# Kernel optimization log

Measured on AMD Instinct MI355X. Metric: run time of the kernel, lower is better.

## Reference

```python
import jax, jax.numpy as jnp
import numpy as np


def setup_inputs() -> dict:
    key = jax.random.key(0)
    ks = jax.random.split(key, 5)
    B, T, C, H, E = 8, 2048, 1024, 2048, 8
    n_layer = 12
    x = jax.random.normal(ks[0], (B, T, C), dtype=jnp.float32)
    w_router = jax.random.normal(ks[1], (C, E), dtype=jnp.float32) * 0.02
    w_c_fc = jax.random.normal(ks[2], (E, C, H), dtype=jnp.float32) * 0.02
    w_gate = jax.random.normal(ks[3], (E, C, H), dtype=jnp.float32) * 0.02
    w_c_proj = jax.random.normal(ks[4], (E, H, C), dtype=jnp.float32) * (0.02 * (2 * n_layer) ** -0.5)
    return {
        "x": x, "w_router": w_router, "w_c_fc": w_c_fc,
        "w_gate": w_gate, "w_c_proj": w_c_proj,
        "top_k": 2, "n_experts": E, "expert_capacity": 640,
    }


def reference(x, w_router, w_c_fc, w_gate, w_c_proj, top_k, n_experts, expert_capacity):
    B, T, C = x.shape
    # ---- router ----
    gate_logits = jnp.einsum('btc,ce->bte', x, w_router)
    gate_probs = jax.nn.softmax(gate_logits, axis=-1)  # (B,T,E)

    # ---- per-batch top-k dispatch (cumsum slot assignment + scatter) ----
    def dispatch(xb, pb):
        # xb: (T,C), pb: (T,E)
        topk_p, topk_i = jax.lax.top_k(pb, top_k)              # (T,k)
        ei = jnp.swapaxes(topk_i, 0, 1).ravel()                # (k*T,) k-major
        oh = jax.nn.one_hot(ei, n_experts, dtype=jnp.int32)    # (k*T,E)
        pos = jnp.cumsum(oh, axis=0) * oh - 1                  # slot within expert
        pos = jnp.swapaxes(pos.reshape(top_k, T, n_experts), 0, 1).max(axis=2)  # (T,k)
        ei = jnp.swapaxes(ei.reshape(top_k, T), 0, 1)          # (T,k)
        buf = jnp.zeros((n_experts, expert_capacity, C), dtype=xb.dtype)
        xr = jnp.repeat(xb, top_k, axis=0)                     # (T*k,C) token-major
        buf = buf.at[ei.ravel(), pos.ravel()].set(xr)          # overflow slots dropped
        return topk_p, pos, ei, buf

    topk_p, pos, ei, buf = jax.vmap(dispatch)(x, gate_probs)   # buf: (B,E,cap,C)

    # ---- batched expert SwiGLU GEMMs ----
    ein = jnp.swapaxes(buf, 0, 1).reshape(n_experts, B * expert_capacity, C)
    h = jnp.einsum('eti,eih->eth', ein, w_c_fc)
    g = jax.nn.silu(jnp.einsum('eti,eih->eth', ein, w_gate))
    o = jnp.einsum('eth,eho->eto', g * h, w_c_proj)
    eo = jnp.swapaxes(o.reshape(n_experts, B, expert_capacity, C), 0, 1)  # (B,E,cap,C)

    # ---- weighted combine gather ----
    def combine(eo_b, i_b, p_b, pr_b):
        sel = eo_b[i_b, p_b]                                   # (T,k,C)
        return jnp.sum(pr_b[..., None] * sel, axis=1)          # (T,C)

    y = jax.vmap(combine)(eo, ei, pos, topk_p)                 # (B,T,C)
    return y
```

## Files before the change

### kernel.cpp

```cpp
#include <hip/hip_runtime.h>
#include <stdint.h>

#define B_   8
#define T_   2048
#define C_   1024
#define H_   2048
#define E_   8
#define CAP_ 640
#define RPE_ (B_*CAP_)
#define BT_  (B_*T_)
#define NE_  2

typedef __attribute__((ext_vector_type(8))) short bf16x8;
typedef __attribute__((ext_vector_type(4))) float f32x4;

static __device__ __forceinline__ unsigned short f2bf(float f){
  union { float f; uint32_t u; } a; a.f = f;
  uint32_t u = a.u;
  uint32_t r = (u + 0x7FFFu + ((u >> 16) & 1u)) >> 16;
  return (unsigned short)r;
}

#define GLD16(gp, lp) __builtin_amdgcn_global_load_lds( \
    (__attribute__((address_space(1))) void*)(gp), \
    (__attribute__((address_space(3))) void*)(lp), 16, 0, 0)

#define SBAR0 __builtin_amdgcn_sched_barrier(0)

#define PHASE(s, vm) do { \
    asm volatile("s_waitcnt vmcnt(" #vm ")" ::: "memory"); \
    SBAR0; \
    __builtin_amdgcn_s_barrier(); \
    SBAR0; \
    COMPUTE(s); \
    SBAR0; \
    __builtin_amdgcn_s_barrier(); \
    SBAR0; \
  } while(0)

__global__ __launch_bounds__(256) void router_kernel(
    const float* __restrict__ x, const float* __restrict__ wr,
    unsigned short* __restrict__ xbf, float* __restrict__ probs2, int* __restrict__ idx2)
{
  int bt = blockIdx.x;
  int tid = threadIdx.x;
  const float4 v = ((const float4*)(x + (size_t)bt*C_))[tid];
  ushort4 u;
  u.x = f2bf(v.x); u.y = f2bf(v.y); u.z = f2bf(v.z); u.w = f2bf(v.w);
  ((ushort4*)(xbf + (size_t)bt*C_))[tid] = u;

  double p[8];
  #pragma unroll
  for (int e=0;e<8;e++) p[e]=0.0;
  const float xv[4] = {v.x, v.y, v.z, v.w};
  #pragma unroll
  for (int j=0;j<4;j++){
    int c = tid*4+j;
    const float* wrow = wr + c*8;
    #pragma unroll
    for (int e=0;e<8;e++) p[e] += (double)xv[j] * (double)wrow[e];
  }
  __shared__ double red[8][256];
  #pragma unroll
  for (int e=0;e<8;e++) red[e][tid] = p[e];
  __syncthreads();
  for (int s=128; s>0; s>>=1){
    if (tid < s){
      #pragma unroll
      for (int e=0;e<8;e++) red[e][tid] += red[e][tid+s];
    }
    __syncthreads();
  }
  if (tid==0){
    double lg[8];
    #pragma unroll
    for (int e=0;e<8;e++) lg[e]=red[e][0];
    double mx = lg[0];
    #pragma unroll
    for (int e=1;e<8;e++) if (lg[e]>mx) mx=lg[e];
    double s=0.0, ex[8];
    #pragma unroll
    for (int e=0;e<8;e++){ ex[e]=exp(lg[e]-mx); s+=ex[e]; }
    int i1=0; double b1=ex[0];
    #pragma unroll
    for (int e=1;e<8;e++) if (ex[e]>b1){ b1=ex[e]; i1=e; }
    int i2=-1; double b2=-1.0;
    #pragma unroll
    for (int e=0;e<8;e++) if (e!=i1 && ex[e]>b2){ b2=ex[e]; i2=e; }
    probs2[bt*2+0] = (float)(b1/s);
    probs2[bt*2+1] = (float)(b2/s);
    idx2[bt*2+0] = i1;
    idx2[bt*2+1] = i2;
  }
}

__global__ __launch_bounds__(256) void transp_fcg_kernel(
    const float* __restrict__ fc, const float* __restrict__ gate,
    unsigned short* __restrict__ dst)
{
  __shared__ float t[32][33];
  int e = blockIdx.z;
  int n0 = blockIdx.x*32, k0 = blockIdx.y*32;
  int tx = threadIdx.x & 31, ty = threadIdx.x >> 5;
  #pragma unroll
  for (int sel=0; sel<2; ++sel){
    const float* s = (sel ? gate : fc) + ((size_t)e*C_ + k0)*H_ + n0;
    #pragma unroll
    for (int i=0;i<32;i+=8) t[ty+i][tx] = s[(size_t)(ty+i)*H_ + tx];
    __syncthreads();
    #pragma unroll
    for (int i=0;i<32;i+=8){
      int jj = ty+i;
      int drow = n0*2 + ((jj & 16) << 1) + sel*16 + (jj & 15);
      dst[((size_t)e*4096 + drow)*1024 + k0 + tx] = f2bf(t[tx][jj]);
    }
    __syncthreads();
  }
}

__global__ __launch_bounds__(256) void transp_kernel(
    const float* __restrict__ src, unsigned short* __restrict__ dst, int K, int N)
{
  __shared__ float t[32][33];
  int e = blockIdx.z;
  int n0 = blockIdx.x*32, k0 = blockIdx.y*32;
  int tx = threadIdx.x & 31, ty = threadIdx.x >> 5;
  const float* s = src + ((size_t)e*K + k0)*N + n0;
  #pragma unroll
  for (int i=0;i<32;i+=8) t[ty+i][tx] = s[(size_t)(ty+i)*N + tx];
  __syncthreads();
  unsigned short* d = dst + ((size_t)e*N + n0)*K + k0;
  #pragma unroll
  for (int i=0;i<32;i+=8) d[(size_t)(ty+i)*K + tx] = f2bf(t[tx][ty+i]);
}

__global__ void scan_kernel(const int* __restrict__ idx2, int* __restrict__ pos, int* __restrict__ cnt)
{
  int b = blockIdx.x, lane = threadIdx.x;
  unsigned long long below = (lane == 0) ? 0ull : (~0ull >> (64 - lane));
  int base = 0;
  for (int k=0;k<2;k++){
    for (int c0=0;c0<T_;c0+=64){
      int t = c0 + lane;
      int e = idx2[((b*T_ + t)<<1) + k];
      unsigned long long mym = 0; int addv = 0;
      #pragma unroll
      for (int ee=0; ee<8; ++ee){
        unsigned long long m = __ballot(e == ee);
        if (ee == e) mym = m;
        if (lane == ee) addv = __popcll(m);
      }
      int mybase = __shfl(base, e, 64);
      pos[((b*T_+t)<<1)+k] = mybase + __popcll(mym & below);
      base += addv;
    }
  }
  if (lane < 8) cnt[b*8 + lane] = (base < CAP_) ? base : CAP_;
}

__global__ void offsets_kernel(const int* __restrict__ cnt, int* __restrict__ off, int* __restrict__ Me)
{
  int e = threadIdx.x;
  if (e < 8){
    int s = 0;
    for (int b=0;b<8;b++){ off[e*8+b] = s; s += cnt[b*8+e]; }
    Me[e] = s;
  }
}

__global__ void fill_kernel(const int* __restrict__ idx2, const int* __restrict__ pos,
                            const int* __restrict__ off, const float* __restrict__ probs2,
                            int* __restrict__ token_src, float* __restrict__ row_prob)
{
  int a = blockIdx.x*256 + threadIdx.x;
  if (a >= BT_*2) return;
  int bt = a >> 1, k = a & 1;
  int b = bt >> 11;
  int e = idx2[bt*2+k];
  int p = pos[bt*2+k];
  if (p < CAP_){
    int r = e*RPE_ + off[e*8+b] + p;
    token_src[r] = bt;
    row_prob[r] = probs2[bt*2+k];
  }
}

__global__ __launch_bounds__(256) void gemm1_kernel(
    const unsigned short* __restrict__ xbf,
    const unsigned short* __restrict__ wifcg,
    const int* __restrict__ token_src,
    const int* __restrict__ Me,
    unsigned short* __restrict__ act,
    int e0)
{
  const int ez = blockIdx.z, e = e0 + ez, mt = blockIdx.y, nt = blockIdx.x;
  const int M = Me[e];
  if (mt*128 >= M) return;

  __shared__ __align__(16) unsigned char lds[65536];

  const int tid = threadIdx.x;
  const int w = tid >> 6, l = tid & 63;
  const int wrow = w >> 1, wcol = w & 1;

  size_t aBase[2], bBase[2];
  #pragma unroll
  for (int j=0;j<2;++j){
    int idx = j*256 + tid;
    int r = idx >> 2, c = idx & 3;
    int sc = c ^ ((r >> 1) & 3);
    int tok = token_src[e*RPE_ + mt*128 + r];
    aBase[j] = (size_t)tok*2048u + (unsigned)(sc*16);
    bBase[j] = ((size_t)(ez*4096 + nt*128 + r))*2048u + (unsigned)(sc*16);
  }
  const unsigned char* gA = (const unsigned char*)xbf;
  const unsigned char* gB = (const unsigned char*)wifcg;

  unsigned rdA[4], rdB[4];
  const int g = l >> 4;
  #pragma unroll
  for (int f=0; f<4; ++f){
    int ra = wrow*64 + f*16 + (l & 15);
    rdA[f] = (unsigned)(ra*64 + ((g ^ ((ra>>1)&3)) << 4));
    int rb = wcol*64 + f*16 + (l & 15);
    rdB[f] = (unsigned)(32768 + rb*64 + ((g ^ ((rb>>1)&3)) << 4));
  }

  f32x4 acc[4][4];
  #pragma unroll
  for (int i=0;i<4;i++)
    #pragma unroll
    for (int j=0;j<4;j++) acc[i][j] = (f32x4){0.f,0.f,0.f,0.f};

  #define STAGE(s) do { \
    unsigned slot_ = ((unsigned)(s)&3u)*8192u; \
    unsigned kb_ = (unsigned)(s)*64u; \
    GLD16(gA + aBase[0] + kb_, lds + slot_ + 0*4096 + w*1024); \
    GLD16(gA + aBase[1] + kb_, lds + slot_ + 1*4096 + w*1024); \
    GLD16(gB + bBase[0] + kb_, lds + 32768 + slot_ + 0*4096 + w*1024); \
    GLD16(gB + bBase[1] + kb_, lds + 32768 + slot_ + 1*4096 + w*1024); \
  } while(0)

  #define COMPUTE(s) do { \
    unsigned slot_ = ((unsigned)(s)&3u)*8192u; \
    bf16x8 afr[4], bfr[4]; \
    _Pragma("unroll") \
    for (int f=0; f<4; ++f) afr[f] = *(const bf16x8*)(lds + slot_ + rdA[f]); \
    _Pragma("unroll") \
    for (int f=0; f<4; ++f) bfr[f] = *(const bf16x8*)(lds + slot_ + rdB[f]); \
    __builtin_amdgcn_s_setprio(1); \
    _Pragma("unroll") \
    for (int fm=0; fm<4; ++fm) \
      _Pragma("unroll") \
      for (int fn=0; fn<4; ++fn) \
        acc[fm][fn] = __builtin_amdgcn_mfma_f32_16x16x32_bf16(afr[fm], bfr[fn], acc[fm][fn], 0,0,0); \
    __builtin_amdgcn_s_setprio(0); \
  } while(0)

  STAGE(0); STAGE(1); STAGE(2);
  for (int s = 0; s < 29; ++s){
    STAGE(s+3);
    PHASE(s, 12);
  }
  PHASE(29, 8);
  PHASE(30, 4);
  PHASE(31, 0);

  #undef STAGE
  #undef COMPUTE

  #pragma unroll
  for (int fm=0; fm<4; ++fm){
    #pragma unroll
    for (int t=0; t<2; ++t){
      f32x4 h = acc[fm][2*t], gg = acc[fm][2*t+1];
      #pragma unroll
      for (int r=0; r<4; ++r){
        int row = mt*128 + wrow*64 + fm*16 + (l>>4)*4 + r;
        int col = nt*64 + wcol*32 + t*16 + (l & 15);
        float gv = gg[r];
        float a = (gv / (1.f + __expf(-gv))) * h[r];
        act[((size_t)ez*RPE_ + row)*(size_t)H_ + col] = f2bf(a);
      }
    }
  }
}

__global__ __launch_bounds__(256) void gemm2_kernel(
    const unsigned short* __restrict__ act,
    const unsigned short* __restrict__ wprojT,
    const int* __restrict__ token_src,
    const float* __restrict__ row_prob,
    const int* __restrict__ Me,
    float* __restrict__ y,
    int e0)
{
  const int ez = blockIdx.z, e = e0 + ez, mt = blockIdx.y, nt = blockIdx.x;
  const int M = Me[e];
  if (mt*128 >= M) return;

  __shared__ __align__(16) unsigned char lds[65536];

  const int tid = threadIdx.x;
  const int w = tid >> 6, l = tid & 63;
  const int wrow = w >> 1, wcol = w & 1;

  size_t aBase[2], bBase[2];
  #pragma unroll
  for (int j=0;j<2;++j){
    int idx = j*256 + tid;
    int r = idx >> 2, c = idx & 3;
    int sc = c ^ ((r >> 1) & 3);
    aBase[j] = ((size_t)(ez*RPE_ + mt*128 + r))*4096u + (unsigned)(sc*16);
    bBase[j] = ((size_t)(ez*C_ + nt*128 + r))*4096u + (unsigned)(sc*16);
  }
  const unsigned char* gA = (const unsigned char*)act;
  const unsigned char* gB = (const unsigned char*)wprojT;

  unsigned rdA[4], rdB[4];
  const int g = l >> 4;
  #pragma unroll
  for (int f=0; f<4; ++f){
    int ra = wrow*64 + f*16 + (l & 15);
    rdA[f] = (unsigned)(ra*64 + ((g ^ ((ra>>1)&3)) << 4));
    int rb = wcol*64 + f*16 + (l & 15);
    rdB[f] = (unsigned)(32768 + rb*64 + ((g ^ ((rb>>1)&3)) << 4));
  }

  f32x4 acc[4][4];
  #pragma unroll
  for (int i=0;i<4;i++)
    #pragma unroll
    for (int j=0;j<4;j++) acc[i][j] = (f32x4){0.f,0.f,0.f,0.f};

  #define STAGE(s) do { \
    unsigned slot_ = ((unsigned)(s)&3u)*8192u; \
    unsigned kb_ = (unsigned)(s)*64u; \
    GLD16(gA + aBase[0] + kb_, lds + slot_ + 0*4096 + w*1024); \
    GLD16(gA + aBase[1] + kb_, lds + slot_ + 1*4096 + w*1024); \
    GLD16(gB + bBase[0] + kb_, lds + 32768 + slot_ + 0*4096 + w*1024); \
    GLD16(gB + bBase[1] + kb_, lds + 32768 + slot_ + 1*4096 + w*1024); \
  } while(0)

  #define COMPUTE(s) do { \
    unsigned slot_ = ((unsigned)(s)&3u)*8192u; \
    bf16x8 afr[4], bfr[4]; \
    _Pragma("unroll") \
    for (int f=0; f<4; ++f) afr[f] = *(const bf16x8*)(lds + slot_ + rdA[f]); \
    _Pragma("unroll") \
    for (int f=0; f<4; ++f) bfr[f] = *(const bf16x8*)(lds + slot_ + rdB[f]); \
    __builtin_amdgcn_s_setprio(1); \
    _Pragma("unroll") \
    for (int fm=0; fm<4; ++fm) \
      _Pragma("unroll") \
      for (int fn=0; fn<4; ++fn) \
        acc[fm][fn] = __builtin_amdgcn_mfma_f32_16x16x32_bf16(afr[fm], bfr[fn], acc[fm][fn], 0,0,0); \
    __builtin_amdgcn_s_setprio(0); \
  } while(0)

  STAGE(0); STAGE(1); STAGE(2);
  for (int s = 0; s < 61; ++s){
    STAGE(s+3);
    PHASE(s, 12);
  }
  PHASE(61, 8);
  PHASE(62, 4);
  PHASE(63, 0);

  #undef STAGE
  #undef COMPUTE

  #pragma unroll
  for (int fm=0; fm<4; ++fm){
    #pragma unroll
    for (int r=0; r<4; ++r){
      int rloc = mt*128 + wrow*64 + fm*16 + (l>>4)*4 + r;
      if (rloc < M){
        int bt  = token_src[e*RPE_ + rloc];
        float p = row_prob[e*RPE_ + rloc];
        float* yrow = y + (size_t)bt*C_;
        #pragma unroll
        for (int fn=0; fn<4; ++fn){
          int col = nt*128 + wcol*64 + fn*16 + (l & 15);
          atomicAdd(yrow + col, p * acc[fm][fn][r]);
        }
      }
    }
  }
}

extern "C" void kernel_launch(void* const* d_in, const int* in_sizes, int n_in,
                              void* d_out, int out_size, void* d_ws, size_t ws_size,
                              hipStream_t stream)
{
  const float* x   = (const float*)d_in[0];
  const float* wr  = (const float*)d_in[1];
  const float* wfc = (const float*)d_in[2];
  const float* wg  = (const float*)d_in[3];
  const float* wpj = (const float*)d_in[4];
  float* y = (float*)d_out;

  unsigned char* ws = (unsigned char*)d_ws;
  const size_t szXBF  = (size_t)BT_*C_*2;
  const size_t szFCGc = (size_t)NE_*4096*1024*2;
  const size_t szWPc  = (size_t)NE_*C_*H_*2;
  const size_t szFCGa = (size_t)E_*4096*1024*2;
  const size_t szWPa  = (size_t)E_*C_*H_*2;
  const size_t szACT  = (size_t)NE_*RPE_*H_*2;
  const size_t szMISC = 3*131072 + 2*(size_t)E_*RPE_*4 + 1024;

  const size_t need_small = szXBF + szFCGc + szWPc + szACT + szMISC;
  const size_t need_big   = szXBF + szFCGa + szWPa + szACT + szMISC;
  if (ws_size < need_small) return;
  const bool big = (ws_size >= need_big);

  const size_t szFCG = big ? szFCGa : szFCGc;
  const size_t szWP  = big ? szWPa  : szWPc;

  size_t oXBF = 0;
  size_t oFCG = oXBF + szXBF;
  size_t oWP  = oFCG + szFCG;
  size_t oACT = oWP  + szWP;
  size_t oM   = oACT + szACT;

  unsigned short* xbf    = (unsigned short*)(ws + oXBF);
  unsigned short* wifcg  = (unsigned short*)(ws + oFCG);
  unsigned short* wprojT = (unsigned short*)(ws + oWP);
  unsigned short* actc   = (unsigned short*)(ws + oACT);

  float* probs2    = (float*)(ws + oM);
  int*   idx2      = (int*)(ws + oM + 1*131072);
  int*   pos       = (int*)(ws + oM + 2*131072);
  int*   token_src = (int*)(ws + oM + 3*131072);
  float* row_prob  = (float*)(ws + oM + 3*131072 + (size_t)E_*RPE_*4);
  int*   cnt       = (int*)(ws + oM + 3*131072 + 2*(size_t)E_*RPE_*4);
  int*   off       = cnt + 64;
  int*   Me        = off + 64;

  hipMemsetAsync(y, 0, (size_t)out_size*4, stream);
  hipMemsetAsync(token_src, 0, (size_t)E_*RPE_*4, stream);

  router_kernel<<<BT_, 256, 0, stream>>>(x, wr, xbf, probs2, idx2);
  scan_kernel<<<B_, 64, 0, stream>>>(idx2, pos, cnt);
  offsets_kernel<<<1, 64, 0, stream>>>(cnt, off, Me);
  fill_kernel<<<(BT_*2+255)/256, 256, 0, stream>>>(idx2, pos, off, probs2, token_src, row_prob);

  if (big){
    transp_fcg_kernel<<<dim3(H_/32, C_/32, E_), 256, 0, stream>>>(wfc, wg, wifcg);
    transp_kernel<<<dim3(C_/32, H_/32, E_), 256, 0, stream>>>(wpj, wprojT, H_, C_);
  }

  for (int e0 = 0; e0 < E_; e0 += NE_){
    unsigned short* wfcg_c = wifcg;
    unsigned short* wpj_c  = wprojT;
    if (big){
      wfcg_c = wifcg  + (size_t)e0*4096*1024;
      wpj_c  = wprojT + (size_t)e0*C_*H_;
    } else {
      transp_fcg_kernel<<<dim3(H_/32, C_/32, NE_), 256, 0, stream>>>(
          wfc + (size_t)e0*C_*H_, wg + (size_t)e0*C_*H_, wifcg);
      transp_kernel<<<dim3(C_/32, H_/32, NE_), 256, 0, stream>>>(
          wpj + (size_t)e0*H_*C_, wprojT, H_, C_);
    }
    gemm1_kernel<<<dim3(4096/128, RPE_/128, NE_), 256, 0, stream>>>(
        xbf, wfcg_c, token_src, Me, actc, e0);
    gemm2_kernel<<<dim3(C_/128, RPE_/128, NE_), 256, 0, stream>>>(
        actc, wpj_c, token_src, row_prob, Me, y, e0);
  }
}
```

Before: 900.0 us.

## Enlarge expert GEMM tiles to 256x256 with 8 waves and double-buffered LDS

Both expert GEMM kernels move from 128x128 tiles with 4 waves and a 4-slot BK=32 ring to 256x256 tiles with 8 waves, BK=64 and two 64KB LDS buffers. Each K-step is split into four quadrant phases that interleave the next tile's loads with MFMA work. The goal is more operand reuse per byte loaded and less barrier overhead per MFMA. In exchange it uses 128KB of LDS and many more accumulator registers per block, which may limit occupancy and leave partially filled M tiles on experts with few tokens.

```diff
diff --git a/kernel.cpp b/kernel.cpp
--- a/kernel.cpp
+++ b/kernel.cpp
@@ -25,18 +25,53 @@
     (__attribute__((address_space(1))) void*)(gp), \
     (__attribute__((address_space(3))) void*)(lp), 16, 0, 0)
 
-#define SBAR0 __builtin_amdgcn_sched_barrier(0)
-
-#define PHASE(s, vm) do { \
-    asm volatile("s_waitcnt vmcnt(" #vm ")" ::: "memory"); \
-    SBAR0; \
-    __builtin_amdgcn_s_barrier(); \
-    SBAR0; \
-    COMPUTE(s); \
-    SBAR0; \
-    __builtin_amdgcn_s_barrier(); \
-    SBAR0; \
-  } while(0)
+#define VMW(N) asm volatile("s_waitcnt vmcnt(" #N ")" ::: "memory")
+#define FENCE  asm volatile("" ::: "memory")
+
+#define PHASE(AH, BH, STG_STMT, WAIT_STMT) do { \
+  bf16x8 afr[2][4], bfr[2][2]; \
+  _Pragma("unroll") \
+  for (int ks=0; ks<2; ++ks){ \
+    _Pragma("unroll") \
+    for (int f=0; f<4; ++f) \
+      afr[ks][f] = *(const bf16x8*)(bufc + (AH)*16384u + aRow + (unsigned)f*2048u + cc[ks]); \
+    _Pragma("unroll") \
+    for (int n=0; n<2; ++n) \
+      bfr[ks][n] = *(const bf16x8*)(bufc + 32768u + (BH)*16384u + bRow + (unsigned)n*2048u + cc[ks]); \
+  } \
+  STG_STMT; \
+  WAIT_STMT; \
+  FENCE; \
+  __builtin_amdgcn_s_barrier(); \
+  __builtin_amdgcn_sched_barrier(0); \
+  __builtin_amdgcn_s_setprio(1); \
+  _Pragma("unroll") \
+  for (int ks=0; ks<2; ++ks) \
+    _Pragma("unroll") \
+    for (int f=0; f<4; ++f) \
+      _Pragma("unroll") \
+      for (int n=0; n<2; ++n) \
+        acc[(AH)*2+(BH)][f][n] = __builtin_amdgcn_mfma_f32_16x16x32_bf16( \
+            afr[ks][f], bfr[ks][n], acc[(AH)*2+(BH)][f][n], 0,0,0); \
+  __builtin_amdgcn_s_setprio(0); \
+  __builtin_amdgcn_sched_barrier(0); \
+  FENCE; \
+  __builtin_amdgcn_s_barrier(); \
+  FENCE; \
+} while(0)
+
+#define STG_A(H, T1) do { \
+  unsigned kb_ = (unsigned)(T1)*128u; \
+  unsigned db_ = ((unsigned)(T1)&1u)*65536u + (H)*16384u; \
+  GLD16(pA##H##0 + kb_, lds + db_ + d0); \
+  GLD16(pA##H##1 + kb_, lds + db_ + 8192u + d0); \
+} while(0)
+#define STG_B(H, T1) do { \
+  unsigned kb_ = (unsigned)(T1)*128u; \
+  unsigned db_ = ((unsigned)(T1)&1u)*65536u + 32768u + (H)*16384u; \
+  GLD16(pB##H##0 + kb_, lds + db_ + d0); \
+  GLD16(pB##H##1 + kb_, lds + db_ + 8192u + d0); \
+} while(0)
 
 __global__ __launch_bounds__(256) void router_kernel(
     const float* __restrict__ x, const float* __restrict__ wr,
@@ -185,7 +220,7 @@
   }
 }
 
-__global__ __launch_bounds__(256) void gemm1_kernel(
+__global__ __launch_bounds__(512, 2) void gemm1_kernel(
     const unsigned short* __restrict__ xbf,
     const unsigned short* __restrict__ wifcg,
     const int* __restrict__ token_src,
@@ -195,98 +230,85 @@
 {
   const int ez = blockIdx.z, e = e0 + ez, mt = blockIdx.y, nt = blockIdx.x;
   const int M = Me[e];
-  if (mt*128 >= M) return;
-
-  __shared__ __align__(16) unsigned char lds[65536];
+  if (mt*256 >= M) return;
+
+  __shared__ __align__(16) unsigned char lds[131072];
 
   const int tid = threadIdx.x;
   const int w = tid >> 6, l = tid & 63;
-  const int wrow = w >> 1, wcol = w & 1;
-
-  size_t aBase[2], bBase[2];
-  #pragma unroll
-  for (int j=0;j<2;++j){
-    int idx = j*256 + tid;
-    int r = idx >> 2, c = idx & 3;
-    int sc = c ^ ((r >> 1) & 3);
-    int tok = token_src[e*RPE_ + mt*128 + r];
-    aBase[j] = (size_t)tok*2048u + (unsigned)(sc*16);
-    bBase[j] = ((size_t)(ez*4096 + nt*128 + r))*2048u + (unsigned)(sc*16);
-  }
+  const int wm = w >> 2, wn = w & 3;
+  const int l15 = l & 15, g0 = l >> 4;
+  const unsigned d0 = (unsigned)tid * 16u;
+
+  const int srow0 = tid >> 3, c0 = tid & 7;
+  const unsigned scb = (unsigned)((c0 ^ (srow0 & 7)) * 16);
   const unsigned char* gA = (const unsigned char*)xbf;
   const unsigned char* gB = (const unsigned char*)wifcg;
-
-  unsigned rdA[4], rdB[4];
-  const int g = l >> 4;
-  #pragma unroll
-  for (int f=0; f<4; ++f){
-    int ra = wrow*64 + f*16 + (l & 15);
-    rdA[f] = (unsigned)(ra*64 + ((g ^ ((ra>>1)&3)) << 4));
-    int rb = wcol*64 + f*16 + (l & 15);
-    rdB[f] = (unsigned)(32768 + rb*64 + ((g ^ ((rb>>1)&3)) << 4));
-  }
-
-  f32x4 acc[4][4];
-  #pragma unroll
-  for (int i=0;i<4;i++)
-    #pragma unroll
-    for (int j=0;j<4;j++) acc[i][j] = (f32x4){0.f,0.f,0.f,0.f};
-
-  #define STAGE(s) do { \
-    unsigned slot_ = ((unsigned)(s)&3u)*8192u; \
-    unsigned kb_ = (unsigned)(s)*64u; \
-    GLD16(gA + aBase[0] + kb_, lds + slot_ + 0*4096 + w*1024); \
-    GLD16(gA + aBase[1] + kb_, lds + slot_ + 1*4096 + w*1024); \
-    GLD16(gB + bBase[0] + kb_, lds + 32768 + slot_ + 0*4096 + w*1024); \
-    GLD16(gB + bBase[1] + kb_, lds + 32768 + slot_ + 1*4096 + w*1024); \
-  } while(0)
-
-  #define COMPUTE(s) do { \
-    unsigned slot_ = ((unsigned)(s)&3u)*8192u; \
-    bf16x8 afr[4], bfr[4]; \
-    _Pragma("unroll") \
-    for (int f=0; f<4; ++f) afr[f] = *(const bf16x8*)(lds + slot_ + rdA[f]); \
-    _Pragma("unroll") \
-    for (int f=0; f<4; ++f) bfr[f] = *(const bf16x8*)(lds + slot_ + rdB[f]); \
-    __builtin_amdgcn_s_setprio(1); \
-    _Pragma("unroll") \
-    for (int fm=0; fm<4; ++fm) \
-      _Pragma("unroll") \
-      for (int fn=0; fn<4; ++fn) \
-        acc[fm][fn] = __builtin_amdgcn_mfma_f32_16x16x32_bf16(afr[fm], bfr[fn], acc[fm][fn], 0,0,0); \
-    __builtin_amdgcn_s_setprio(0); \
-  } while(0)
-
-  STAGE(0); STAGE(1); STAGE(2);
-  for (int s = 0; s < 29; ++s){
-    STAGE(s+3);
-    PHASE(s, 12);
-  }
-  PHASE(29, 8);
-  PHASE(30, 4);
-  PHASE(31, 0);
-
-  #undef STAGE
-  #undef COMPUTE
-
-  #pragma unroll
-  for (int fm=0; fm<4; ++fm){
-    #pragma unroll
-    for (int t=0; t<2; ++t){
-      f32x4 h = acc[fm][2*t], gg = acc[fm][2*t+1];
-      #pragma unroll
-      for (int r=0; r<4; ++r){
-        int row = mt*128 + wrow*64 + fm*16 + (l>>4)*4 + r;
-        int col = nt*64 + wcol*32 + t*16 + (l & 15);
-        float gv = gg[r];
-        float a = (gv / (1.f + __expf(-gv))) * h[r];
-        act[((size_t)ez*RPE_ + row)*(size_t)H_ + col] = f2bf(a);
+  const int abase = e*RPE_ + mt*256;
+  const unsigned char* pA00 = gA + (size_t)token_src[abase +       srow0]*2048u + scb;
+  const unsigned char* pA01 = gA + (size_t)token_src[abase +  64 + srow0]*2048u + scb;
+  const unsigned char* pA10 = gA + (size_t)token_src[abase + 128 + srow0]*2048u + scb;
+  const unsigned char* pA11 = gA + (size_t)token_src[abase + 192 + srow0]*2048u + scb;
+  const size_t bbase = (size_t)(ez*4096 + nt*256 + srow0);
+  const unsigned char* pB00 = gB + (bbase +   0)*2048u + scb;
+  const unsigned char* pB01 = gB + (bbase +  64)*2048u + scb;
+  const unsigned char* pB10 = gB + (bbase + 128)*2048u + scb;
+  const unsigned char* pB11 = gB + (bbase + 192)*2048u + scb;
+
+  const unsigned aRow = (unsigned)((wm*64 + l15) * 128);
+  const unsigned bRow = (unsigned)((wn*32 + l15) * 128);
+  unsigned cc[2];
+  cc[0] = (unsigned)(((0*4 + g0) ^ (l15 & 7)) * 16);
+  cc[1] = (unsigned)(((1*4 + g0) ^ (l15 & 7)) * 16);
+
+  f32x4 acc[4][4][2];
+  #pragma unroll
+  for (int p=0;p<4;++p)
+    #pragma unroll
+    for (int f=0;f<4;++f)
+      #pragma unroll
+      for (int n=0;n<2;++n) acc[p][f][n] = (f32x4){0.f,0.f,0.f,0.f};
+
+  STG_A(0,0); STG_B(0,0); STG_B(1,0); STG_A(1,0);
+  VMW(4);
+  FENCE; __builtin_amdgcn_s_barrier(); FENCE;
+
+  const int NT = 16;
+  for (int t = 0; t < NT-1; ++t){
+    const unsigned char* bufc = lds + (unsigned)(t&1)*65536u;
+    PHASE(0,0, STG_A(0,t+1), VMW(4));
+    PHASE(0,1, STG_B(0,t+1), VMW(4));
+    PHASE(1,0, STG_B(1,t+1), (void)0);
+    PHASE(1,1, STG_A(1,t+1), VMW(4));
+  }
+  {
+    const unsigned char* bufc = lds + (unsigned)((NT-1)&1)*65536u;
+    PHASE(0,0, (void)0, VMW(2));
+    PHASE(0,1, (void)0, VMW(0));
+    PHASE(1,0, (void)0, (void)0);
+    PHASE(1,1, (void)0, (void)0);
+  }
+
+  const int r4 = (l >> 4) * 4;
+  #pragma unroll
+  for (int p=0;p<4;++p){
+    const int ah = p>>1, bh = p&1;
+    #pragma unroll
+    for (int f=0;f<4;++f){
+      const int grow = mt*256 + ah*128 + wm*64 + f*16 + r4;
+      const int hcol = nt*128 + bh*64 + wn*16 + l15;
+      #pragma unroll
+      for (int r=0;r<4;++r){
+        float h = acc[p][f][0][r];
+        float gv = acc[p][f][1][r];
+        float a = (gv / (1.f + __expf(-gv))) * h;
+        act[((size_t)ez*RPE_ + grow + r)*(size_t)H_ + hcol] = f2bf(a);
       }
     }
   }
 }
 
-__global__ __launch_bounds__(256) void gemm2_kernel(
+__global__ __launch_bounds__(512, 2) void gemm2_kernel(
     const unsigned short* __restrict__ act,
     const unsigned short* __restrict__ wprojT,
     const int* __restrict__ token_src,
@@ -297,92 +319,81 @@
 {
   const int ez = blockIdx.z, e = e0 + ez, mt = blockIdx.y, nt = blockIdx.x;
   const int M = Me[e];
-  if (mt*128 >= M) return;
-
-  __shared__ __align__(16) unsigned char lds[65536];
+  if (mt*256 >= M) return;
+
+  __shared__ __align__(16) unsigned char lds[131072];
 
   const int tid = threadIdx.x;
   const int w = tid >> 6, l = tid & 63;
-  const int wrow = w >> 1, wcol = w & 1;
-
-  size_t aBase[2], bBase[2];
-  #pragma unroll
-  for (int j=0;j<2;++j){
-    int idx = j*256 + tid;
-    int r = idx >> 2, c = idx & 3;
-    int sc = c ^ ((r >> 1) & 3);
-    aBase[j] = ((size_t)(ez*RPE_ + mt*128 + r))*4096u + (unsigned)(sc*16);
-    bBase[j] = ((size_t)(ez*C_ + nt*128 + r))*4096u + (unsigned)(sc*16);
-  }
+  const int wm = w >> 2, wn = w & 3;
+  const int l15 = l & 15, g0 = l >> 4;
+  const unsigned d0 = (unsigned)tid * 16u;
+
+  const int srow0 = tid >> 3, c0 = tid & 7;
+  const unsigned scb = (unsigned)((c0 ^ (srow0 & 7)) * 16);
   const unsigned char* gA = (const unsigned char*)act;
   const unsigned char* gB = (const unsigned char*)wprojT;
-
-  unsigned rdA[4], rdB[4];
-  const int g = l >> 4;
-  #pragma unroll
-  for (int f=0; f<4; ++f){
-    int ra = wrow*64 + f*16 + (l & 15);
-    rdA[f] = (unsigned)(ra*64 + ((g ^ ((ra>>1)&3)) << 4));
-    int rb = wcol*64 + f*16 + (l & 15);
-    rdB[f] = (unsigned)(32768 + rb*64 + ((g ^ ((rb>>1)&3)) << 4));
-  }
-
-  f32x4 acc[4][4];
-  #pragma unroll
-  for (int i=0;i<4;i++)
-    #pragma unroll
-    for (int j=0;j<4;j++) acc[i][j] = (f32x4){0.f,0.f,0.f,0.f};
-
-  #define STAGE(s) do { \
-    unsigned slot_ = ((unsigned)(s)&3u)*8192u; \
-    unsigned kb_ = (unsigned)(s)*64u; \
-    GLD16(gA + aBase[0] + kb_, lds + slot_ + 0*4096 + w*1024); \
-    GLD16(gA + aBase[1] + kb_, lds + slot_ + 1*4096 + w*1024); \
-    GLD16(gB + bBase[0] + kb_, lds + 32768 + slot_ + 0*4096 + w*1024); \
-    GLD16(gB + bBase[1] + kb_, lds + 32768 + slot_ + 1*4096 + w*1024); \
-  } while(0)
-
-  #define COMPUTE(s) do { \
-    unsigned slot_ = ((unsigned)(s)&3u)*8192u; \
-    bf16x8 afr[4], bfr[4]; \
-    _Pragma("unroll") \
-    for (int f=0; f<4; ++f) afr[f] = *(const bf16x8*)(lds + slot_ + rdA[f]); \
-    _Pragma("unroll") \
-    for (int f=0; f<4; ++f) bfr[f] = *(const bf16x8*)(lds + slot_ + rdB[f]); \
-    __builtin_amdgcn_s_setprio(1); \
-    _Pragma("unroll") \
-    for (int fm=0; fm<4; ++fm) \
-      _Pragma("unroll") \
-      for (int fn=0; fn<4; ++fn) \
-        acc[fm][fn] = __builtin_amdgcn_mfma_f32_16x16x32_bf16(afr[fm], bfr[fn], acc[fm][fn], 0,0,0); \
-    __builtin_amdgcn_s_setprio(0); \
-  } while(0)
-
-  STAGE(0); STAGE(1); STAGE(2);
-  for (int s = 0; s < 61; ++s){
-    STAGE(s+3);
-    PHASE(s, 12);
-  }
-  PHASE(61, 8);
-  PHASE(62, 4);
-  PHASE(63, 0);
-
-  #undef STAGE
-  #undef COMPUTE
-
-  #pragma unroll
-  for (int fm=0; fm<4; ++fm){
-    #pragma unroll
-    for (int r=0; r<4; ++r){
-      int rloc = mt*128 + wrow*64 + fm*16 + (l>>4)*4 + r;
-      if (rloc < M){
-        int bt  = token_src[e*RPE_ + rloc];
-        float p = row_prob[e*RPE_ + rloc];
-        float* yrow = y + (size_t)bt*C_;
-        #pragma unroll
-        for (int fn=0; fn<4; ++fn){
-          int col = nt*128 + wcol*64 + fn*16 + (l & 15);
-          atomicAdd(yrow + col, p * acc[fm][fn][r]);
+  const size_t abase = (size_t)(ez*RPE_ + mt*256 + srow0);
+  const unsigned char* pA00 = gA + (abase +   0)*4096u + scb;
+  const unsigned char* pA01 = gA + (abase +  64)*4096u + scb;
+  const unsigned char* pA10 = gA + (abase + 128)*4096u + scb;
+  const unsigned char* pA11 = gA + (abase + 192)*4096u + scb;
+  const size_t bbase = (size_t)(ez*C_ + nt*256 + srow0);
+  const unsigned char* pB00 = gB + (bbase +   0)*4096u + scb;
+  const unsigned char* pB01 = gB + (bbase +  64)*4096u + scb;
+  const unsigned char* pB10 = gB + (bbase + 128)*4096u + scb;
+  const unsigned char* pB11 = gB + (bbase + 192)*4096u + scb;
+
+  const unsigned aRow = (unsigned)((wm*64 + l15) * 128);
+  const unsigned bRow = (unsigned)((wn*32 + l15) * 128);
+  unsigned cc[2];
+  cc[0] = (unsigned)(((0*4 + g0) ^ (l15 & 7)) * 16);
+  cc[1] = (unsigned)(((1*4 + g0) ^ (l15 & 7)) * 16);
+
+  f32x4 acc[4][4][2];
+  #pragma unroll
+  for (int p=0;p<4;++p)
+    #pragma unroll
+    for (int f=0;f<4;++f)
+      #pragma unroll
+      for (int n=0;n<2;++n) acc[p][f][n] = (f32x4){0.f,0.f,0.f,0.f};
+
+  STG_A(0,0); STG_B(0,0); STG_B(1,0); STG_A(1,0);
+  VMW(4);
+  FENCE; __builtin_amdgcn_s_barrier(); FENCE;
+
+  const int NT = 32;
+  for (int t = 0; t < NT-1; ++t){
+    const unsigned char* bufc = lds + (unsigned)(t&1)*65536u;
+    PHASE(0,0, STG_A(0,t+1), VMW(4));
+    PHASE(0,1, STG_B(0,t+1), VMW(4));
+    PHASE(1,0, STG_B(1,t+1), (void)0);
+    PHASE(1,1, STG_A(1,t+1), VMW(4));
+  }
+  {
+    const unsigned char* bufc = lds + (unsigned)((NT-1)&1)*65536u;
+    PHASE(0,0, (void)0, VMW(2));
+    PHASE(0,1, (void)0, VMW(0));
+    PHASE(1,0, (void)0, (void)0);
+    PHASE(1,1, (void)0, (void)0);
+  }
+
+  const int r4 = (l >> 4) * 4;
+  #pragma unroll
+  for (int p=0;p<4;++p){
+    const int ah = p>>1, bh = p&1;
+    #pragma unroll
+    for (int f=0;f<4;++f){
+      #pragma unroll
+      for (int r=0;r<4;++r){
+        const int rloc = mt*256 + ah*128 + wm*64 + f*16 + r4 + r;
+        if (rloc < M){
+          const int bt = token_src[e*RPE_ + rloc];
+          const float pp = row_prob[e*RPE_ + rloc];
+          float* yrow = y + (size_t)bt*C_;
+          const int colb = nt*256 + bh*128 + wn*32 + l15;
+          atomicAdd(yrow + colb,      pp * acc[p][f][0][r]);
+          atomicAdd(yrow + colb + 16, pp * acc[p][f][1][r]);
         }
       }
     }
@@ -462,9 +473,9 @@
       transp_kernel<<<dim3(C_/32, H_/32, NE_), 256, 0, stream>>>(
           wpj + (size_t)e0*H_*C_, wprojT, H_, C_);
     }
-    gemm1_kernel<<<dim3(4096/128, RPE_/128, NE_), 256, 0, stream>>>(
+    gemm1_kernel<<<dim3(4096/256, RPE_/256, NE_), 512, 0, stream>>>(
         xbf, wfcg_c, token_src, Me, actc, e0);
-    gemm2_kernel<<<dim3(C_/128, RPE_/128, NE_), 256, 0, stream>>>(
+    gemm2_kernel<<<dim3(C_/256, RPE_/256, NE_), 512, 0, stream>>>(
         actc, wpj_c, token_src, row_prob, Me, y, e0);
   }
 }
```

Result: slower. 930.7 us (+3.4%).
